# Kernel tuning notes

Hardware: AMD Instinct MI355X
Metric: run time of the kernel (lower is better)

## Reference

```python
import jax, jax.numpy as jnp
import numpy as np

B, S, E, H, FF = 2, 2048, 768, 12, 3072
D = E // H
EPS = 1e-5


def setup_inputs() -> dict:
    key = jax.random.key(0)
    ks = jax.random.split(key, 12)
    sc = lambda n: 1.0 / np.sqrt(n)
    return {
        "x": jax.random.normal(ks[0], (B, S, E), jnp.float32),
        "wq": jax.random.normal(ks[1], (E, E), jnp.float32) * sc(E),
        "wk": jax.random.normal(ks[2], (E, E), jnp.float32) * sc(E),
        "wv": jax.random.normal(ks[3], (E, E), jnp.float32) * sc(E),
        "wo": jax.random.normal(ks[4], (E, E), jnp.float32) * sc(E),
        "bo": jax.random.normal(ks[5], (E,), jnp.float32) * 0.02,
        "w1": jax.random.normal(ks[6], (FF, E), jnp.float32) * sc(E),
        "b1": jax.random.normal(ks[7], (FF,), jnp.float32) * 0.02,
        "w2": jax.random.normal(ks[8], (E, FF), jnp.float32) * sc(FF),
        "b2": jax.random.normal(ks[9], (E,), jnp.float32) * 0.02,
        "gamma": jnp.ones((E,), jnp.float32),
        "beta": jnp.zeros((E,), jnp.float32),
    }


def _layernorm(x, g, b):
    mu = jnp.mean(x, axis=-1, keepdims=True)
    var = jnp.mean(jnp.square(x - mu), axis=-1, keepdims=True)
    return (x - mu) * jax.lax.rsqrt(var + EPS) * g + b


def reference(x, wq, wk, wv, wo, bo, w1, b1, w2, b2, gamma, beta):
    res = x
    xn = _layernorm(x, gamma, beta)
    # Q/K/V projections (torch Linear: y = x @ W.T), split into heads
    q = (xn @ wq.T).reshape(B, S, H, D)
    k = (xn @ wk.T).reshape(B, S, H, D)
    v = (xn @ wv.T).reshape(B, S, H, D)
    scale = jnp.sqrt(jnp.float32(D))
    scores = jnp.einsum("bqhd,bkhd->bhqk", q, k) / scale  # [B,H,S,S]
    causal = jnp.tril(jnp.ones((S, S), bool))
    scores = jnp.where(causal, scores, -jnp.inf)
    w = jax.nn.softmax(scores, axis=-1)
    attn = jnp.einsum("bhqk,bkhd->bqhd", w, v).reshape(B, S, E)
    attn = attn @ wo.T + bo
    res = res + attn
    y = _layernorm(res, gamma, beta)  # NOTE: same LayerNorm params reused (as in source)
    h = jax.nn.gelu(y @ w1.T + b1, approximate=False)  # nn.GELU default is exact erf
    ffn = h @ w2.T + b2
    return res + ffn
```

## Files before the change

kernel.cpp:

```cpp
#include <hip/hip_runtime.h>
#include <hip/hip_bf16.h>
#include <math.h>

typedef __bf16 bf16_8 __attribute__((ext_vector_type(8)));
typedef __bf16 bf16_4 __attribute__((ext_vector_type(4)));
typedef float f32x4 __attribute__((ext_vector_type(4)));

#define AS1 __attribute__((address_space(1)))
#define AS3 __attribute__((address_space(3)))

__global__ __launch_bounds__(256) void ln_kernel(
    const float* __restrict__ x, const float* __restrict__ g,
    const float* __restrict__ b, __hip_bfloat16* __restrict__ out, int cols) {
  const int row = blockIdx.x;
  const int t = threadIdx.x;
  float loc[3];
  float s = 0.f, s2 = 0.f;
#pragma unroll
  for (int i = 0; i < 3; ++i) {
    float v = x[(size_t)row * cols + t + i * 256];
    loc[i] = v;
    s += v;
    s2 += v * v;
  }
#pragma unroll
  for (int off = 32; off; off >>= 1) {
    s += __shfl_down(s, off);
    s2 += __shfl_down(s2, off);
  }
  __shared__ float red[2][4];
  const int lane = t & 63, w = t >> 6;
  if (lane == 0) {
    red[0][w] = s;
    red[1][w] = s2;
  }
  __syncthreads();
  s = red[0][0] + red[0][1] + red[0][2] + red[0][3];
  s2 = red[1][0] + red[1][1] + red[1][2] + red[1][3];
  const float mu = s / cols;
  const float var = s2 / cols - mu * mu;
  const float rs = rsqrtf(var + 1e-5f);
  __hip_bfloat16* orow = out + (size_t)row * cols;
#pragma unroll
  for (int i = 0; i < 3; ++i) {
    int c = t + i * 256;
    orow[c] = __hip_bfloat16((loc[i] - mu) * rs * g[c] + b[c]);
  }
}

__global__ __launch_bounds__(256) void reduce_ln(
    const float* __restrict__ x, const float* __restrict__ part, int nz,
    const float* __restrict__ bias, const float* __restrict__ g,
    const float* __restrict__ b, float* __restrict__ res,
    __hip_bfloat16* __restrict__ yout) {
  const int row = blockIdx.x;
  const int t = threadIdx.x;
  const size_t zstride = (size_t)4096 * 768;
  float loc[3];
  float s = 0.f, s2 = 0.f;
#pragma unroll
  for (int i = 0; i < 3; ++i) {
    const int c = t + i * 256;
    const size_t off = (size_t)row * 768 + c;
    float v = x[off] + bias[c];
    for (int z = 0; z < nz; ++z) v += part[(size_t)z * zstride + off];
    res[off] = v;
    loc[i] = v;
    s += v;
    s2 += v * v;
  }
#pragma unroll
  for (int off = 32; off; off >>= 1) {
    s += __shfl_down(s, off);
    s2 += __shfl_down(s2, off);
  }
  __shared__ float red[2][4];
  const int lane = t & 63, w = t >> 6;
  if (lane == 0) {
    red[0][w] = s;
    red[1][w] = s2;
  }
  __syncthreads();
  s = red[0][0] + red[0][1] + red[0][2] + red[0][3];
  s2 = red[1][0] + red[1][1] + red[1][2] + red[1][3];
  const float mu = s / 768.f;
  const float var = s2 / 768.f - mu * mu;
  const float rs = rsqrtf(var + 1e-5f);
#pragma unroll
  for (int i = 0; i < 3; ++i) {
    const int c = t + i * 256;
    yout[(size_t)row * 768 + c] = __hip_bfloat16((loc[i] - mu) * rs * g[c] + b[c]);
  }
}

__global__ __launch_bounds__(256) void reduce_out(
    const float* __restrict__ part, int nz, const float* __restrict__ bias,
    float* __restrict__ res) {
  const int row = blockIdx.x;
  const int t = threadIdx.x;
  const size_t zstride = (size_t)4096 * 768;
#pragma unroll
  for (int i = 0; i < 3; ++i) {
    const int c = t + i * 256;
    const size_t off = (size_t)row * 768 + c;
    float v = res[off] + bias[c];
    for (int z = 0; z < nz; ++z) v += part[(size_t)z * zstride + off];
    res[off] = v;
  }
}

__global__ __launch_bounds__(256) void cvt_multi(
    const float* __restrict__ sa, const float* __restrict__ sb,
    const float* __restrict__ sc, const float* __restrict__ sd,
    __hip_bfloat16* __restrict__ da, __hip_bfloat16* __restrict__ db,
    __hip_bfloat16* __restrict__ dc, __hip_bfloat16* __restrict__ dd) {
  const float* src;
  __hip_bfloat16* dst;
  if (blockIdx.y == 0) { src = sa; dst = da; }
  else if (blockIdx.y == 1) { src = sb; dst = db; }
  else if (blockIdx.y == 2) { src = sc; dst = dc; }
  else { src = sd; dst = dd; }
  const size_t i = ((size_t)blockIdx.x * 256 + threadIdx.x) * 4;
  float4 f = *(const float4*)(src + i);
  bf16_4 o;
  o[0] = (__bf16)f.x; o[1] = (__bf16)f.y; o[2] = (__bf16)f.z; o[3] = (__bf16)f.w;
  *(bf16_4*)((__bf16*)dst + i) = o;
}

__global__ __launch_bounds__(256) void transpose_v(
    const __hip_bfloat16* __restrict__ v, __hip_bfloat16* __restrict__ vt) {
  const int S = 2048, E = 768, H = 12;
  const int s0 = blockIdx.x * 64;
  const int bh = blockIdx.y;
  const int b = bh / H, h = bh - b * H;
  __shared__ __align__(16) __bf16 T[64 * 72];
  const int tid = threadIdx.x;
#pragma unroll
  for (int u = 0; u < 2; ++u) {
    int i = tid + u * 256;
    int sr = i >> 3, c = i & 7;
    *(bf16_8*)(&T[sr * 72 + c * 8]) =
        *(const bf16_8*)(v + ((size_t)b * S + s0 + sr) * E + h * 64 + c * 8);
  }
  __syncthreads();
#pragma unroll
  for (int u = 0; u < 2; ++u) {
    int i = tid + u * 256;
    int dr = i >> 3, kc = i & 7;
    bf16_8 o;
#pragma unroll
    for (int e = 0; e < 8; ++e) {
      int k = 32 * (kc >> 2) + 16 * (e >> 2) + 4 * (kc & 3) + (e & 3);
      o[e] = T[k * 72 + dr];
    }
    *(bf16_8*)(vt + ((size_t)bh * 64 + dr) * S + s0 + kc * 8) = o;
  }
}

template <int MODE, bool BF32>
__global__ __launch_bounds__(256) void gemm_bt(
    const __hip_bfloat16* __restrict__ A, const void* __restrict__ Bx,
    const float* __restrict__ bias, void* __restrict__ out,
    int M, int N, int K, int lda, int ldb, int ldout) {
  constexpr int BM = 128, BN = 128, BK = 64;
  constexpr int LDBP = BF32 ? 72 : BK;
  __shared__ __align__(16) __bf16 As[BM * BK];
  __shared__ __align__(16) __bf16 Bs[BN * LDBP];
  const int tid = threadIdx.x;
  const int m0 = blockIdx.y * BM;
  const int n0 = blockIdx.x * BN;
  const int wave = tid >> 6;
  const int lane = tid & 63;
  const int quad = lane >> 4;
  const int l16 = lane & 15;
  const int wm = (wave & 1) * 64;
  const int wn = (wave >> 1) * 64;

  int kbase = 0, kcnt = K;
  if constexpr (MODE == 2 || MODE == 3) {
    kcnt = K / gridDim.z;
    kbase = blockIdx.z * kcnt;
  }

  const int srow = lane >> 3;
  const int scol = ((lane & 7) ^ (srow & 7)) * 8;
  const __hip_bfloat16* Ap = A + (size_t)(m0 + wave * 8 + srow) * lda + kbase + scol;
  const __hip_bfloat16* Bpb = nullptr;
  const float* Bpf = nullptr;
  if constexpr (BF32)
    Bpf = (const float*)Bx;
  else
    Bpb = (const __hip_bfloat16*)Bx + (size_t)(n0 + wave * 8 + srow) * ldb + kbase + scol;

  f32x4 acc[4][4] = {};

  for (int k0 = 0; k0 < kcnt; k0 += BK) {
    __syncthreads();
#pragma unroll
    for (int u = 0; u < 4; ++u) {
      __builtin_amdgcn_global_load_lds(
          (const AS1 void*)(Ap + (size_t)(u * 32) * lda + k0),
          (AS3 void*)(&As[(u * 32 + wave * 8) * BK]), 16, 0, 0);
      if constexpr (!BF32)
        __builtin_amdgcn_global_load_lds(
            (const AS1 void*)(Bpb + (size_t)(u * 32) * ldb + k0),
            (AS3 void*)(&Bs[(u * 32 + wave * 8) * BK]), 16, 0, 0);
    }
    if constexpr (BF32) {
#pragma unroll
      for (int u = 0; u < 4; ++u) {
        int c = u * 256 + tid;
        int row = c >> 3, kc = c & 7;
        const float* src = Bpf + (size_t)(n0 + row) * ldb + kbase + k0 + kc * 8;
        float4 f0 = *(const float4*)src;
        float4 f1 = *(const float4*)(src + 4);
        bf16_8 bv;
        bv[0] = (__bf16)f0.x; bv[1] = (__bf16)f0.y; bv[2] = (__bf16)f0.z; bv[3] = (__bf16)f0.w;
        bv[4] = (__bf16)f1.x; bv[5] = (__bf16)f1.y; bv[6] = (__bf16)f1.z; bv[7] = (__bf16)f1.w;
        *(bf16_8*)(&Bs[row * LDBP + kc * 8]) = bv;
      }
    }
    __syncthreads();
#pragma unroll
    for (int kk = 0; kk < 2; ++kk) {
      bf16_8 af[4], bfr[4];
#pragma unroll
      for (int i = 0; i < 4; ++i)
        af[i] = *(const bf16_8*)(
            &As[(wm + i * 16 + l16) * BK + (((kk * 4 + quad) ^ (l16 & 7)) * 8)]);
#pragma unroll
      for (int j = 0; j < 4; ++j) {
        if constexpr (BF32)
          bfr[j] = *(const bf16_8*)(&Bs[(wn + j * 16 + l16) * LDBP + kk * 32 + quad * 8]);
        else
          bfr[j] = *(const bf16_8*)(
              &Bs[(wn + j * 16 + l16) * BK + (((kk * 4 + quad) ^ (l16 & 7)) * 8)]);
      }
#pragma unroll
      for (int i = 0; i < 4; ++i)
#pragma unroll
        for (int j = 0; j < 4; ++j)
          acc[i][j] =
              __builtin_amdgcn_mfma_f32_16x16x32_bf16(af[i], bfr[j], acc[i][j], 0, 0, 0);
    }
  }

#pragma unroll
  for (int i = 0; i < 4; ++i) {
#pragma unroll
    for (int j = 0; j < 4; ++j) {
#pragma unroll
      for (int r = 0; r < 4; ++r) {
        const int row = m0 + wm + i * 16 + quad * 4 + r;
        const int col = n0 + wn + j * 16 + l16;
        const float v = acc[i][j][r];
        if constexpr (MODE == 0) {
          const int tsel = n0 / 768;
          const size_t idx = ((size_t)tsel * M + row) * 768 + (col - tsel * 768);
          ((__hip_bfloat16*)out)[idx] = __hip_bfloat16(v);
        } else if constexpr (MODE == 1) {
          float tt = v + bias[col];
          float gl = 0.5f * tt * (1.0f + erff(tt * 0.70710678118654752f));
          ((__hip_bfloat16*)out)[(size_t)row * ldout + col] = __hip_bfloat16(gl);
        } else if constexpr (MODE == 2) {
          float add = v + ((blockIdx.z == 0 && bias) ? bias[col] : 0.f);
          atomicAdd((float*)out + (size_t)row * 768 + col, add);
        } else {
          ((float*)out)[(size_t)blockIdx.z * M * 768 + (size_t)row * 768 + col] = v;
        }
      }
    }
  }
}

__global__ void zero_ctr(int* __restrict__ c) {
  if (threadIdx.x == 0) *c = 0;
}

#define ALDP 72
template <bool PRE_T>
__global__ __launch_bounds__(256) void attn_mfma(
    const __hip_bfloat16* __restrict__ qb, const __hip_bfloat16* __restrict__ kb,
    const __hip_bfloat16* __restrict__ vb, __hip_bfloat16* __restrict__ ob,
    int* __restrict__ ctr) {
  const int S = 2048, H = 12, E = 768;
  const int tid = threadIdx.x;
  const int wave = tid >> 6;
  const int lane = tid & 63;
  const int quad = lane >> 4;
  const int l16 = lane & 15;

  __shared__ __align__(16) __bf16 Ks[2][64 * 64];
  __shared__ __align__(16) __bf16 Vt[2][64 * 64];
  __shared__ int task;
  __bf16* ep = &Ks[0][0] + wave * 16 * ALDP;

  const int srow8 = lane >> 3;
  const int csrc = ((lane & 7) ^ srow8) * 8;

  const float SCL = 0.18033688011112042f;

  for (;;) {
    if (tid == 0) task = atomicAdd(ctr, 1);
    __syncthreads();
    const int t = task;
    if (t >= 24 * 32) return;
    const int qblk = 31 - (t / 24);
    const int bh = t - (t / 24) * 24;
    const int b = bh / H, h = bh - b * H;
    const int q0 = qblk * 64;
    const int qw = q0 + wave * 16;
    const size_t base = (size_t)b * S * E + (size_t)h * 64;

    auto STAGE = [&](int kts, int buf) {
      const int k0s = kts * 64;
#pragma unroll
      for (int u = 0; u < 2; ++u) {
        const int trow = wave * 16 + u * 8;
        __builtin_amdgcn_global_load_lds(
            (const AS1 void*)(kb + base + (size_t)(k0s + trow + srow8) * E + csrc),
            (AS3 void*)(&Ks[buf][trow * 64]), 16, 0, 0);
        if constexpr (PRE_T)
          __builtin_amdgcn_global_load_lds(
              (const AS1 void*)(vb + ((size_t)(bh * 64 + trow + srow8)) * S + k0s + csrc),
              (AS3 void*)(&Vt[buf][trow * 64]), 16, 0, 0);
      }
      if constexpr (!PRE_T) {
#pragma unroll
        for (int u = 0; u < 2; ++u) {
          int i = tid + u * 256;
          int kr = i & 63, dq = i >> 6;
          bf16_8 vv = *(const bf16_8*)(vb + base + (size_t)(k0s + kr) * E + dq * 8);
          const int c = 32 * (kr >> 5) + 8 * ((kr >> 2) & 3) + 4 * ((kr >> 4) & 1) + (kr & 3);
#pragma unroll
          for (int j = 0; j < 8; ++j) {
            int drow = dq * 8 + j;
            Vt[buf][drow * 64 + (((c >> 3) ^ (drow & 7)) * 8) + (c & 7)] = vv[j];
          }
        }
      }
    };

    bf16_8 qf[2];
#pragma unroll
    for (int s = 0; s < 2; ++s)
      qf[s] = *(const bf16_8*)(qb + base + (size_t)(qw + l16) * E + s * 32 + quad * 8);

    f32x4 o[4] = {};
    float mq = -1e30f, lq = 0.f;

    STAGE(0, 0);
    __syncthreads();
    int cur = 0;

    for (int kt = 0; kt <= qblk; ++kt) {
      const int k0 = kt * 64;
      if (kt < qblk) STAGE(kt + 1, cur ^ 1);

      f32x4 sc[4] = {};
      __builtin_amdgcn_s_setprio(1);
#pragma unroll
      for (int jj = 0; jj < 4; ++jj)
#pragma unroll
        for (int s = 0; s < 2; ++s) {
          bf16_8 kf = *(const bf16_8*)(
              &Ks[cur][(jj * 16 + l16) * 64 + (((s * 4 + quad) ^ (l16 & 7)) * 8)]);
          sc[jj] = __builtin_amdgcn_mfma_f32_16x16x32_bf16(kf, qf[s], sc[jj], 0, 0, 0);
        }
      __builtin_amdgcn_s_setprio(0);

#pragma unroll
      for (int jj = 0; jj < 4; ++jj)
#pragma unroll
        for (int r = 0; r < 4; ++r) sc[jj][r] *= SCL;
      if (kt == qblk) {
#pragma unroll
        for (int jj = 0; jj < 4; ++jj)
#pragma unroll
          for (int r = 0; r < 4; ++r)
            if ((k0 + jj * 16 + quad * 4 + r) > (qw + l16)) sc[jj][r] = -1e30f;
      }
      float mj[4];
#pragma unroll
      for (int jj = 0; jj < 4; ++jj)
        mj[jj] = fmaxf(fmaxf(sc[jj][0], sc[jj][1]), fmaxf(sc[jj][2], sc[jj][3]));
      float mx = fmaxf(fmaxf(mj[0], mj[1]), fmaxf(mj[2], mj[3]));
      mx = fmaxf(mx, __shfl_xor(mx, 16));
      mx = fmaxf(mx, __shfl_xor(mx, 32));
      const float mn = fmaxf(mq, mx);
      const float corr = exp2f(mq - mn);
      mq = mn;
      float sj[4];
#pragma unroll
      for (int jj = 0; jj < 4; ++jj) {
#pragma unroll
        for (int r = 0; r < 4; ++r) sc[jj][r] = exp2f(sc[jj][r] - mn);
        sj[jj] = (sc[jj][0] + sc[jj][1]) + (sc[jj][2] + sc[jj][3]);
      }
      float sum = (sj[0] + sj[1]) + (sj[2] + sj[3]);
      sum += __shfl_xor(sum, 16);
      sum += __shfl_xor(sum, 32);
      lq = lq * corr + sum;
#pragma unroll
      for (int nt2 = 0; nt2 < 4; ++nt2)
#pragma unroll
        for (int r = 0; r < 4; ++r) o[nt2][r] *= corr;

      bf16_8 pf[2];
#pragma unroll
      for (int s = 0; s < 2; ++s)
#pragma unroll
        for (int r = 0; r < 4; ++r) {
          pf[s][r] = (__bf16)sc[2 * s][r];
          pf[s][4 + r] = (__bf16)sc[2 * s + 1][r];
        }

      __builtin_amdgcn_s_setprio(1);
#pragma unroll
      for (int s = 0; s < 2; ++s)
#pragma unroll
        for (int dt = 0; dt < 4; ++dt) {
          bf16_8 vf = *(const bf16_8*)(
              &Vt[cur][(dt * 16 + l16) * 64 + (((s * 4 + quad) ^ (l16 & 7)) * 8)]);
          o[dt] = __builtin_amdgcn_mfma_f32_16x16x32_bf16(vf, pf[s], o[dt], 0, 0, 0);
        }
      __builtin_amdgcn_s_setprio(0);

      __syncthreads();
      cur ^= 1;
    }

    const float inv = 1.f / lq;
#pragma unroll
    for (int dt = 0; dt < 4; ++dt) {
      bf16_4 o4;
#pragma unroll
      for (int r = 0; r < 4; ++r) o4[r] = (__bf16)(o[dt][r] * inv);
      *(bf16_4*)(&ep[l16 * ALDP + dt * 16 + quad * 4]) = o4;
    }
#pragma unroll
    for (int u = 0; u < 2; ++u) {
      int j = lane + u * 64;
      int ql = j >> 3, ch = j & 7;
      bf16_8 ov = *(const bf16_8*)(&ep[ql * ALDP + ch * 8]);
      *(bf16_8*)(ob + base + (size_t)(qw + ql) * E + ch * 8) = ov;
    }
  }
}

extern "C" void kernel_launch(void* const* d_in, const int* in_sizes, int n_in,
                              void* d_out, int out_size, void* d_ws, size_t ws_size,
                              hipStream_t stream) {
  const int Bv = 2, S = 2048, E = 768, FF = 3072;
  const int M = Bv * S;
  const size_t ME = (size_t)M * E;
  const size_t EE = (size_t)E * E;
  const size_t EF = (size_t)E * FF;

  const float* x = (const float*)d_in[0];
  const float* wq = (const float*)d_in[1];
  const float* wk = (const float*)d_in[2];
  const float* wv = (const float*)d_in[3];
  const float* wo = (const float*)d_in[4];
  const float* bo = (const float*)d_in[5];
  const float* w1 = (const float*)d_in[6];
  const float* b1 = (const float*)d_in[7];
  const float* w2 = (const float*)d_in[8];
  const float* b2 = (const float*)d_in[9];
  const float* gamma = (const float*)d_in[10];
  const float* beta = (const float*)d_in[11];

  int* ctr = (int*)d_ws;
  __hip_bfloat16* slot = (__hip_bfloat16*)((char*)d_ws + 256);
  __hip_bfloat16* s0 = slot;
  __hip_bfloat16* s1 = slot + ME;
  __hip_bfloat16* s4 = slot + 4 * ME;
  __hip_bfloat16* s5 = slot + 5 * ME;
  float* pp = (float*)(slot + 5 * ME + 2 * EF);
  __hip_bfloat16* vt = (__hip_bfloat16*)pp;
  float* res = (float*)d_out;

  const size_t need_mid = 256 + (5 * ME + 2 * EF) * sizeof(__hip_bfloat16);
  const size_t need_full = need_mid + 4 * ME * sizeof(float);
  const bool full = ws_size >= need_full;
  const bool mid = ws_size >= need_mid;

  cvt_multi<<<dim3(EE / 1024, 4), 256, 0, stream>>>(
      wq, wk, wv, wo, s4, s4 + EE, s4 + 2 * EE, s4 + 3 * EE);
  if (mid)
    cvt_multi<<<dim3(EF / 1024, 2), 256, 0, stream>>>(
        w1, w2, nullptr, nullptr, s5, s5 + EF, nullptr, nullptr);
  ln_kernel<<<M, 256, 0, stream>>>(x, gamma, beta, s0, E);
  gemm_bt<0, false><<<dim3(18, 32), 256, 0, stream>>>(s0, s4, nullptr, s1, M, 2304, E, E, E, 0);
  zero_ctr<<<1, 64, 0, stream>>>(ctr);
  if (full) {
    transpose_v<<<dim3(32, 24), 256, 0, stream>>>(s1 + 2 * ME, vt);
    attn_mfma<true><<<768, 256, 0, stream>>>(s1, s1 + ME, vt, s0, ctr);
  } else {
    attn_mfma<false><<<768, 256, 0, stream>>>(s1, s1 + ME, s1 + 2 * ME, s0, ctr);
  }

  if (full) {
    gemm_bt<3, false><<<dim3(6, 32, 4), 256, 0, stream>>>(
        s0, s4 + 3 * EE, nullptr, pp, M, E, E, E, E, 0);
    reduce_ln<<<M, 256, 0, stream>>>(x, pp, 4, bo, gamma, beta, res, s0);
    gemm_bt<1, false><<<dim3(24, 32), 256, 0, stream>>>(s0, s5, b1, s1, M, FF, E, E, E, FF);
    gemm_bt<3, false><<<dim3(6, 32, 4), 256, 0, stream>>>(
        s1, s5 + EF, nullptr, pp, M, E, FF, FF, FF, 0);
    reduce_out<<<M, 256, 0, stream>>>(pp, 4, b2, res);
  } else {
    hipMemcpyAsync(d_out, x, ME * sizeof(float), hipMemcpyDeviceToDevice, stream);
    gemm_bt<2, false><<<dim3(6, 32, 2), 256, 0, stream>>>(
        s0, s4 + 3 * EE, bo, res, M, E, E, E, E, 0);
    ln_kernel<<<M, 256, 0, stream>>>(res, gamma, beta, s0, E);
    if (mid) {
      gemm_bt<1, false><<<dim3(24, 32), 256, 0, stream>>>(s0, s5, b1, s1, M, FF, E, E, E, FF);
      gemm_bt<2, false><<<dim3(6, 32, 4), 256, 0, stream>>>(
          s1, s5 + EF, b2, res, M, E, FF, FF, FF, 0);
    } else {
      gemm_bt<1, true><<<dim3(24, 32), 256, 0, stream>>>(s0, w1, b1, s1, M, FF, E, E, E, FF);
      cvt_multi<<<dim3(EF / 1024, 1), 256, 0, stream>>>(
          w2, nullptr, nullptr, nullptr, s0, nullptr, nullptr, nullptr);
      gemm_bt<2, false><<<dim3(6, 32, 4), 256, 0, stream>>>(
          s1, s0, b2, res, M, E, FF, FF, FF, 0);
    }
  }
}
```

Baseline: 310.6 us.

## Split long causal attention query blocks across two KV halves with combine kernel

Query blocks 16-31 now have their KV range split into two halves that run as separate tasks. Each half writes unnormalised fp32 partial outputs plus running max and sum to the workspace, and a new combine kernel merges them with a log-sum-exp rescale. Tasks are ordered by a constant table that interleaves long and short pieces, so the persistent work queue balances better and the tail shrinks. The cost is extra fp32 partial traffic, one more kernel launch, and more blocks launched.

```diff
diff --git a/kernel.cpp b/kernel.cpp
--- a/kernel.cpp
+++ b/kernel.cpp
@@ -278,11 +278,20 @@
 }
 
 #define ALDP 72
-template <bool PRE_T>
+__device__ __constant__ signed char UQ[48] = {
+    31, 31, 30, 15, 30, 29, 29, 28, 14, 28, 27, 27, 26, 13, 26, 25,
+    25, 24, 12, 24, 23, 23, 22, 11, 22, 21, 21, 20, 10, 20, 19, 19,
+    18, 9, 18, 17, 17, 16, 8, 16, 7, 6, 5, 4, 3, 2, 1, 0};
+__device__ __constant__ signed char UP[48] = {
+    0, 1, 1, 2, 0, 0, 1, 1, 2, 0, 0, 1, 1, 2, 0, 0,
+    1, 1, 2, 0, 0, 1, 1, 2, 0, 0, 1, 1, 2, 0, 0, 1,
+    1, 2, 0, 0, 1, 1, 2, 0, 2, 2, 2, 2, 2, 2, 2, 2};
+
+template <bool PRE_T, bool SPLIT>
 __global__ __launch_bounds__(256) void attn_mfma(
     const __hip_bfloat16* __restrict__ qb, const __hip_bfloat16* __restrict__ kb,
     const __hip_bfloat16* __restrict__ vb, __hip_bfloat16* __restrict__ ob,
-    int* __restrict__ ctr) {
+    float* __restrict__ po, float* __restrict__ pml, int* __restrict__ ctr) {
   const int S = 2048, H = 12, E = 768;
   const int tid = threadIdx.x;
   const int wave = tid >> 6;
@@ -297,20 +306,32 @@
 
   const int srow8 = lane >> 3;
   const int csrc = ((lane & 7) ^ srow8) * 8;
-
   const float SCL = 0.18033688011112042f;
+  const int NTASK = SPLIT ? 24 * 48 : 24 * 32;
 
   for (;;) {
     if (tid == 0) task = atomicAdd(ctr, 1);
     __syncthreads();
     const int t = task;
-    if (t >= 24 * 32) return;
-    const int qblk = 31 - (t / 24);
-    const int bh = t - (t / 24) * 24;
+    if (t >= NTASK) return;
+    int qblk, part, bh;
+    if constexpr (SPLIT) {
+      const int unit = t / 24;
+      bh = t - unit * 24;
+      qblk = UQ[unit];
+      part = UP[unit];
+    } else {
+      qblk = 31 - (t / 24);
+      bh = t - (t / 24) * 24;
+      part = 2;
+    }
     const int b = bh / H, h = bh - b * H;
     const int q0 = qblk * 64;
     const int qw = q0 + wave * 16;
     const size_t base = (size_t)b * S * E + (size_t)h * 64;
+    const int mid = (qblk + 1) >> 1;
+    const int kbgn = (part == 1) ? mid : 0;
+    const int kend = (part == 0) ? mid : qblk + 1;
 
     auto STAGE = [&](int kts, int buf) {
       const int k0s = kts * 64;
@@ -349,13 +370,13 @@
     f32x4 o[4] = {};
     float mq = -1e30f, lq = 0.f;
 
-    STAGE(0, 0);
+    STAGE(kbgn, 0);
     __syncthreads();
     int cur = 0;
 
-    for (int kt = 0; kt <= qblk; ++kt) {
+    for (int kt = kbgn; kt < kend; ++kt) {
       const int k0 = kt * 64;
-      if (kt < qblk) STAGE(kt + 1, cur ^ 1);
+      if (kt + 1 < kend) STAGE(kt + 1, cur ^ 1);
 
       f32x4 sc[4] = {};
       __builtin_amdgcn_s_setprio(1);
@@ -430,21 +451,72 @@
       cur ^= 1;
     }
 
-    const float inv = 1.f / lq;
-#pragma unroll
-    for (int dt = 0; dt < 4; ++dt) {
-      bf16_4 o4;
-#pragma unroll
-      for (int r = 0; r < 4; ++r) o4[r] = (__bf16)(o[dt][r] * inv);
-      *(bf16_4*)(&ep[l16 * ALDP + dt * 16 + quad * 4]) = o4;
-    }
-#pragma unroll
-    for (int u = 0; u < 2; ++u) {
-      int j = lane + u * 64;
-      int ql = j >> 3, ch = j & 7;
-      bf16_8 ov = *(const bf16_8*)(&ep[ql * ALDP + ch * 8]);
-      *(bf16_8*)(ob + base + (size_t)(qw + ql) * E + ch * 8) = ov;
-    }
+    if (SPLIT && part != 2) {
+      const int cidx = bh * 16 + (qblk - 16);
+      float* poT = po + (size_t)cidx * 8192 + part * 4096;
+      const int ql = wave * 16 + l16;
+#pragma unroll
+      for (int dt = 0; dt < 4; ++dt)
+#pragma unroll
+        for (int r = 0; r < 4; ++r)
+          poT[(dt * 16 + quad * 4 + r) * 64 + ql] = o[dt][r];
+      if (quad == 0) {
+        pml[(size_t)cidx * 256 + part * 128 + ql] = mq;
+        pml[(size_t)cidx * 256 + part * 128 + 64 + ql] = lq;
+      }
+    } else {
+      const float inv = 1.f / lq;
+#pragma unroll
+      for (int dt = 0; dt < 4; ++dt) {
+        bf16_4 o4;
+#pragma unroll
+        for (int r = 0; r < 4; ++r) o4[r] = (__bf16)(o[dt][r] * inv);
+        *(bf16_4*)(&ep[l16 * ALDP + dt * 16 + quad * 4]) = o4;
+      }
+#pragma unroll
+      for (int u = 0; u < 2; ++u) {
+        int j = lane + u * 64;
+        int ql = j >> 3, ch = j & 7;
+        bf16_8 ov = *(const bf16_8*)(&ep[ql * ALDP + ch * 8]);
+        *(bf16_8*)(ob + base + (size_t)(qw + ql) * E + ch * 8) = ov;
+      }
+    }
+  }
+}
+
+__global__ __launch_bounds__(256) void attn_combine(
+    const float* __restrict__ po, const float* __restrict__ pml,
+    __hip_bfloat16* __restrict__ ob) {
+  const int S = 2048, H = 12, E = 768;
+  const int cidx = blockIdx.x;
+  const int bh = cidx / 16;
+  const int qblk = 16 + (cidx - bh * 16);
+  const int b = bh / H, h = bh - b * H;
+  const int q0 = qblk * 64;
+  const size_t base = (size_t)b * S * E + (size_t)h * 64;
+  const float* P0 = po + (size_t)cidx * 8192;
+  const float* P1 = P0 + 4096;
+  const float* ML = pml + (size_t)cidx * 256;
+
+  __shared__ float a1[64], a2[64], dn[64];
+  const int t = threadIdx.x;
+  if (t < 64) {
+    const float m1 = ML[t], l1 = ML[64 + t];
+    const float m2 = ML[128 + t], l2 = ML[192 + t];
+    const float ms = fmaxf(m1, m2);
+    const float e1 = exp2f(m1 - ms), e2 = exp2f(m2 - ms);
+    a1[t] = e1;
+    a2[t] = e2;
+    dn[t] = 1.f / (e1 * l1 + e2 * l2);
+  }
+  __syncthreads();
+  const int d = t & 63;
+  const int qg = t >> 6;
+#pragma unroll
+  for (int i = 0; i < 16; ++i) {
+    const int q = qg + i * 4;
+    const float v = (a1[q] * P0[d * 64 + q] + a2[q] * P1[d * 64 + q]) * dn[q];
+    ob[base + (size_t)(q0 + q) * E + d] = __hip_bfloat16(v);
   }
 }
 
@@ -478,6 +550,8 @@
   __hip_bfloat16* s5 = slot + 5 * ME;
   float* pp = (float*)(slot + 5 * ME + 2 * EF);
   __hip_bfloat16* vt = (__hip_bfloat16*)pp;
+  float* po = (float*)((char*)pp + ME * sizeof(__hip_bfloat16));
+  float* pml = po + (size_t)384 * 8192;
   float* res = (float*)d_out;
 
   const size_t need_mid = 256 + (5 * ME + 2 * EF) * sizeof(__hip_bfloat16);
@@ -495,9 +569,11 @@
   zero_ctr<<<1, 64, 0, stream>>>(ctr);
   if (full) {
     transpose_v<<<dim3(32, 24), 256, 0, stream>>>(s1 + 2 * ME, vt);
-    attn_mfma<true><<<768, 256, 0, stream>>>(s1, s1 + ME, vt, s0, ctr);
+    attn_mfma<true, true><<<1024, 256, 0, stream>>>(s1, s1 + ME, vt, s0, po, pml, ctr);
+    attn_combine<<<384, 256, 0, stream>>>(po, pml, s0);
   } else {
-    attn_mfma<false><<<768, 256, 0, stream>>>(s1, s1 + ME, s1 + 2 * ME, s0, ctr);
+    attn_mfma<false, false><<<768, 256, 0, stream>>>(
+        s1, s1 + ME, s1 + 2 * ME, s0, nullptr, nullptr, ctr);
   }
 
   if (full) {
```

Result: slower. 328.7 us (+5.9%).
